# Performance work log

Hardware: AMD Instinct MI355X
Metric: run time of the kernel (lower is better)

Reference implementation:

```python
import jax, jax.numpy as jnp
import numpy as np

B, N, F_IN, F_OUT, T, E, K = 8, 1024, 32, 64, 24, 16384, 3


def setup_inputs() -> dict:
    key = jax.random.key(0)
    ks = jax.random.split(key, 9)
    return {
        "x": jax.random.normal(ks[0], (B, N, F_IN, T), jnp.float32),
        "edge_index": jax.random.randint(ks[1], (2, E), 0, N),
        "edge_weight": jax.random.uniform(ks[2], (E,), jnp.float32),
        # attention params (xavier-ish scale)
        "Ve": jax.random.normal(ks[3], (T, T), jnp.float32) * 0.2,
        "be": jax.random.normal(ks[4], (1, T, T), jnp.float32) * 0.2,
        "Vs": jax.random.normal(ks[5], (N, N), jnp.float32) * 0.03,
        "bs": jax.random.normal(ks[6], (1, N, N), jnp.float32) * 0.03,
        # ChebConv: K linear layers (no bias) + shared bias
        "cheb_W": jax.random.normal(ks[7], (K, F_IN, F_OUT), jnp.float32) * (1.0 / np.sqrt(F_IN)),
        "cheb_b": jnp.zeros((F_OUT,), jnp.float32),
        # 1x1 residual Conv2d(F_IN -> F_OUT): weight (F_OUT, F_IN), bias (F_OUT,)
        "res_W": jax.random.normal(ks[8], (F_OUT, F_IN), jnp.float32) * (1.0 / np.sqrt(F_IN)),
        "res_b": jnp.zeros((F_OUT,), jnp.float32),
    }


def _cheb_conv(x, row, col, w, Wk, b):
    """PyG-style ChebConv applied to a batch of graphs sharing edges.
    x: (BT, N, Fin). Scaled Laplacian with lambda_max=2 reduces to
    L_hat = -D^{-1/2} A D^{-1/2} with zero diagonal (self-loops removed).
    """
    n = x.shape[1]
    w = jnp.where(row == col, jnp.zeros_like(w), w)  # remove_self_loops
    deg = jnp.zeros((n,), x.dtype).at[row].add(w)
    dis = jnp.where(deg > 0, jax.lax.rsqrt(jnp.where(deg > 0, deg, 1.0)), 0.0)
    norm = -dis[row] * w * dis[col]  # (E,)

    def prop(z):  # z: (BT, N, F) -> L_hat @ z
        msg = norm[None, :, None] * z[:, row, :]  # (BT, E, F)
        return jnp.zeros_like(z).at[:, col, :].add(msg)

    Tx0 = x
    out = Tx0 @ Wk[0]
    Tx1 = prop(Tx0)
    out = out + Tx1 @ Wk[1]
    for k in range(2, Wk.shape[0]):  # small fixed K, not a data-dim loop
        Tx2 = 2.0 * prop(Tx1) - Tx0
        out = out + Tx2 @ Wk[k]
        Tx0, Tx1 = Tx1, Tx2
    return out + b


def reference(x, edge_index, edge_weight, Ve, be, Vs, bs, cheb_W, cheb_b, res_W, res_b):
    b_, n, f, t = x.shape
    row, col = edge_index[0], edge_index[1]

    # --- temporal attention: E = softmax(Ve @ sigmoid(X^T X) + be) ---
    x_flat = x.reshape(b_, n * f, t)
    score_t = jnp.einsum('bmt,bmu->btu', x_flat, x_flat)
    E_att = jax.nn.softmax(jnp.einsum('tu,buv->btv', Ve, jax.nn.sigmoid(score_t)) + be, axis=-1)
    x_TA = (x_flat @ E_att).reshape(b_, n, f, t)

    # --- spatial attention: S = softmax(Vs @ sigmoid(X X^T) + bs) ---
    xr = x_TA.reshape(b_, n, f * t)
    score_s = jnp.einsum('bnd,bmd->bnm', xr, xr)
    S_att = jax.nn.softmax(jnp.einsum('nm,bmk->bnk', Vs, jax.nn.sigmoid(score_s)) + bs, axis=-1)
    x_SA = (S_att @ xr).reshape(b_, n, f, t)

    # --- Chebyshev graph conv, batched over all B*T slices at once ---
    xg = x_SA.transpose(0, 3, 1, 2).reshape(b_ * t, n, f)  # (BT, N, Fin)
    x_gcn = _cheb_conv(xg, row, col, edge_weight, cheb_W, cheb_b)
    x_gcn = x_gcn.reshape(b_, t, n, -1).transpose(0, 2, 3, 1)  # (B, N, Fout, T)

    # --- 1x1 residual conv over channel dim ---
    x_res = jnp.einsum('gf,bnft->bngt', res_W, x) + res_b[None, None, :, None]

    return jax.nn.relu(x_gcn + x_res)
```

## Files before the change

### kernel.cpp

```cpp
#include <hip/hip_runtime.h>
#include <math.h>

#define NB 1024
#define FB 32
#define TB 24
#define GB 64
#define BB 8
#define EB 16384
#define MB 32768
#define DB 768
#define BTB 192
#define WSP 6144

typedef __attribute__((ext_vector_type(8))) short sh8;
typedef __attribute__((ext_vector_type(4))) float f32x4;

__device__ __forceinline__ float wsum(float v){
  #pragma unroll
  for (int o = 32; o; o >>= 1) v += __shfl_down(v, o);
  return v;
}
__device__ __forceinline__ float wmax(float v){
  #pragma unroll
  for (int o = 32; o; o >>= 1) v = fmaxf(v, __shfl_down(v, o));
  return v;
}
__device__ __forceinline__ float sigm(float v){ return 1.f / (1.f + expf(-v)); }
__device__ __forceinline__ float b2f(unsigned short u){ unsigned int t = ((unsigned int)u) << 16; return __uint_as_float(t); }
__device__ __forceinline__ unsigned short f2b(float f){
  unsigned int u = __float_as_uint(f);
  u += 0x7fffu + ((u >> 16) & 1u);
  return (unsigned short)(u >> 16);
}
__device__ __forceinline__ void gload16(const void* g, void* l){
  typedef const __attribute__((address_space(1))) unsigned int* gp_t;
  typedef __attribute__((address_space(3))) unsigned int* lp_t;
  __builtin_amdgcn_global_load_lds((gp_t)g, (lp_t)l, 16, 0, 0);
}

__global__ __launch_bounds__(256) void k_score(const float* __restrict__ x,
                                               float* __restrict__ score){
  const int b = blockIdx.y, ch = blockIdx.x;
  __shared__ float xs[512 * 24];
  const float* src = x + (size_t)b * (MB * TB) + (size_t)ch * 512 * 24;
  #pragma unroll
  for (int p = 0; p < 12; ++p){
    int i = p * 256 + threadIdx.x;
    ((float4*)xs)[i] = ((const float4*)src)[i];
  }
  __syncthreads();
  if (threadIdx.x < 192){
    const int t = threadIdx.x >> 3, u0 = (threadIdx.x & 7) * 3;
    float a0 = 0.f, a1 = 0.f, a2 = 0.f;
    for (int m = 0; m < 512; ++m){
      const float xt = xs[m * 24 + t];
      a0 = fmaf(xt, xs[m * 24 + u0 + 0], a0);
      a1 = fmaf(xt, xs[m * 24 + u0 + 1], a1);
      a2 = fmaf(xt, xs[m * 24 + u0 + 2], a2);
    }
    float* sb = score + (size_t)b * 576 + t * 24 + u0;
    atomicAdd(sb + 0, a0); atomicAdd(sb + 1, a1); atomicAdd(sb + 2, a2);
  }
}

__global__ __launch_bounds__(64) void k_eatt(const float* __restrict__ score,
                                             const float* __restrict__ Ve,
                                             const float* __restrict__ be,
                                             float* __restrict__ Eatt){
  const int b = blockIdx.x;
  __shared__ float sg[576], Ar[576], Vel[576], bel[576];
  for (int i = threadIdx.x; i < 576; i += 64){
    sg[i] = sigm(score[(size_t)b * 576 + i]);
    Vel[i] = Ve[i]; bel[i] = be[i];
  }
  __syncthreads();
  for (int i = threadIdx.x; i < 576; i += 64){
    int t = i / 24, v = i % 24;
    float s = 0.f;
    #pragma unroll
    for (int u = 0; u < 24; ++u) s = fmaf(Vel[t*24+u], sg[u*24+v], s);
    Ar[i] = s + bel[i];
  }
  __syncthreads();
  if (threadIdx.x < 24){
    const int t = threadIdx.x;
    float mx = -1e30f;
    #pragma unroll
    for (int v = 0; v < 24; ++v) mx = fmaxf(mx, Ar[t*24+v]);
    float e[24]; float sum = 0.f;
    #pragma unroll
    for (int v = 0; v < 24; ++v){ e[v] = expf(Ar[t*24+v] - mx); sum += e[v]; }
    const float inv = 1.f / sum;
    #pragma unroll
    for (int v = 0; v < 24; ++v) Eatt[(size_t)b * 576 + t*24 + v] = e[v] * inv;
  }
}

__global__ __launch_bounds__(256) void k_xta(const float* __restrict__ x,
                                             const float* __restrict__ Eatt,
                                             unsigned short* __restrict__ xh){
  __shared__ float E[576];
  const int b = blockIdx.x >> 7;
  for (int i = threadIdx.x; i < 576; i += 256) E[i] = Eatt[(size_t)b * 576 + i];
  __syncthreads();
  const size_t m = (size_t)blockIdx.x * 256 + threadIdx.x;
  const float* xr = x + m * TB;
  float in[TB], o[TB];
  #pragma unroll
  for (int q = 0; q < 6; ++q){
    float4 v = *(const float4*)(xr + q * 4);
    in[q*4+0] = v.x; in[q*4+1] = v.y; in[q*4+2] = v.z; in[q*4+3] = v.w;
  }
  #pragma unroll
  for (int v = 0; v < TB; ++v) o[v] = 0.f;
  #pragma unroll
  for (int u = 0; u < TB; ++u){
    const float xv = in[u];
    #pragma unroll
    for (int v = 0; v < TB; ++v) o[v] = fmaf(xv, E[u*24+v], o[v]);
  }
  unsigned int pk[12];
  #pragma unroll
  for (int q = 0; q < 12; ++q)
    pk[q] = (unsigned int)f2b(o[2*q]) | ((unsigned int)f2b(o[2*q+1]) << 16);
  uint4* op = (uint4*)(xh + m * TB);
  op[0] = make_uint4(pk[0], pk[1], pk[2], pk[3]);
  op[1] = make_uint4(pk[4], pk[5], pk[6], pk[7]);
  op[2] = make_uint4(pk[8], pk[9], pk[10], pk[11]);
}

__global__ __launch_bounds__(256) void k_tr(const unsigned short* __restrict__ in,
                                            unsigned short* __restrict__ out){
  const int dt = blockIdx.x, nt = blockIdx.y, b = blockIdx.z;
  __shared__ unsigned short ts[64 * 66];
  const unsigned short* ib = in + (size_t)b * (NB * DB) + (size_t)(nt * 64) * DB + dt * 64;
  #pragma unroll
  for (int p = 0; p < 8; ++p){
    int fl = p * 256 + threadIdx.x;
    int rr = fl >> 5, cc = (fl & 31) * 2;
    unsigned int v = *(const unsigned int*)(ib + (size_t)rr * DB + cc);
    ts[rr * 66 + cc] = (unsigned short)v;
    ts[rr * 66 + cc + 1] = (unsigned short)(v >> 16);
  }
  __syncthreads();
  unsigned short* ob = out + (size_t)b * (NB * DB) + (size_t)(dt * 64) * NB + nt * 64;
  #pragma unroll
  for (int p = 0; p < 16; ++p){
    int fl = p * 256 + threadIdx.x;
    int dd = fl >> 6, nn = fl & 63;
    ob[(size_t)dd * NB + nn] = ts[nn * 66 + dd];
  }
}

template<int EPI>
__global__ __launch_bounds__(256) void k_mgemm(const unsigned short* __restrict__ A,
                                               const unsigned short* __restrict__ B,
                                               unsigned short* __restrict__ C,
                                               int lda, int ldb, int ldc, int Kk, int nbx,
                                               long sA, long sB, long sC){
  __shared__ unsigned short As[2][8192];
  __shared__ unsigned short Bs[2][8192];
  const int d = blockIdx.x;
  const int bz = d & 7;
  const int rr = d >> 3;
  const int bx = rr % nbx, by = rr / nbx;
  A += (size_t)bz * sA; B += (size_t)bz * sB; C += (size_t)bz * sC;
  const int i0 = by * 128, j0 = bx * 128;
  const int tid = threadIdx.x, wave = tid >> 6, lane = tid & 63;
  const int fr = lane & 15, rowb = (lane >> 4) * 4;
  const int wr = (wave >> 1) * 64, wc = (wave & 1) * 64;
  const int srow = tid >> 3;
  const int sko = (((lane & 7) ^ (lane >> 3)) * 8);
  f32x4 acc[4][4];
  #pragma unroll
  for (int m = 0; m < 4; ++m)
    #pragma unroll
    for (int n = 0; n < 4; ++n) acc[m][n] = 0.f;

  auto stage = [&](int buf, int k0){
    #pragma unroll
    for (int it = 0; it < 4; ++it){
      const int r = it * 32 + srow;
      gload16(A + (size_t)(i0 + r) * lda + k0 + sko, &As[buf][(it*4 + wave) * 512]);
      gload16(B + (size_t)(j0 + r) * ldb + k0 + sko, &Bs[buf][(it*4 + wave) * 512]);
    }
  };
  auto compute = [&](int buf){
    #pragma unroll
    for (int kk = 0; kk < 2; ++kk){
      const int ch = kk * 4 + (lane >> 4);
      const int cs = (ch ^ (fr & 7)) * 8;
      sh8 af[4], bfr[4];
      #pragma unroll
      for (int m = 0; m < 4; ++m)
        af[m] = *(const sh8*)&As[buf][(wr + m*16 + fr) * 64 + cs];
      #pragma unroll
      for (int n = 0; n < 4; ++n)
        bfr[n] = *(const sh8*)&Bs[buf][(wc + n*16 + fr) * 64 + cs];
      #pragma unroll
      for (int m = 0; m < 4; ++m)
        #pragma unroll
        for (int n = 0; n < 4; ++n)
          acc[m][n] = __builtin_amdgcn_mfma_f32_16x16x32_bf16(af[m], bfr[n], acc[m][n], 0, 0, 0);
    }
  };

  stage(0, 0);
  asm volatile("s_waitcnt vmcnt(0)" ::: "memory");
  __builtin_amdgcn_s_barrier();
  int cur = 0;
  for (int k0 = 64; k0 < Kk; k0 += 64){
    stage(cur ^ 1, k0);
    compute(cur);
    asm volatile("s_waitcnt vmcnt(0)" ::: "memory");
    __builtin_amdgcn_s_barrier();
    cur ^= 1;
  }
  compute(cur);

  #pragma unroll
  for (int m = 0; m < 4; ++m){
    const int row = i0 + wr + m*16 + rowb;
    #pragma unroll
    for (int n = 0; n < 4; ++n){
      const int colg = j0 + wc + n*16 + fr;
      #pragma unroll
      for (int r = 0; r < 4; ++r){
        float v = acc[m][n][r];
        if (EPI == 1) v = sigm(v);
        C[(size_t)(row + r) * ldc + colg] = f2b(v);
      }
    }
  }
}

__global__ __launch_bounds__(256) void k_softmax_s(const unsigned short* __restrict__ C2h,
                                                   const float* __restrict__ bs,
                                                   unsigned short* __restrict__ Sh){
  const int blk = blockIdx.x;
  const int n = blk & 1023;
  const unsigned short* row = C2h + (size_t)blk * 1024;
  const float* bsr = bs + (size_t)n * 1024;
  const int tid = threadIdx.x;
  uint2 rv = ((const uint2*)row)[tid];
  float4 bb = ((const float4*)bsr)[tid];
  float v0 = b2f((unsigned short)rv.x)         + bb.x;
  float v1 = b2f((unsigned short)(rv.x >> 16)) + bb.y;
  float v2 = b2f((unsigned short)rv.y)         + bb.z;
  float v3 = b2f((unsigned short)(rv.y >> 16)) + bb.w;
  float mx = fmaxf(fmaxf(v0, v1), fmaxf(v2, v3));
  mx = wmax(mx);
  __shared__ float s4[4];
  __shared__ float s4b[4];
  if ((tid & 63) == 0) s4[tid >> 6] = mx;
  __syncthreads();
  mx = fmaxf(fmaxf(s4[0], s4[1]), fmaxf(s4[2], s4[3]));
  float e0 = expf(v0 - mx), e1 = expf(v1 - mx), e2 = expf(v2 - mx), e3 = expf(v3 - mx);
  float sum = wsum(e0 + e1 + e2 + e3);
  if ((tid & 63) == 0) s4b[tid >> 6] = sum;
  __syncthreads();
  sum = s4b[0] + s4b[1] + s4b[2] + s4b[3];
  const float inv = 1.f / sum;
  uint2 ov;
  ov.x = (unsigned int)f2b(e0 * inv) | ((unsigned int)f2b(e1 * inv) << 16);
  ov.y = (unsigned int)f2b(e2 * inv) | ((unsigned int)f2b(e3 * inv) << 16);
  ((uint2*)(Sh + (size_t)blk * 1024))[tid] = ov;
}

__global__ __launch_bounds__(256) void k_t0n(const unsigned short* __restrict__ xSAh,
                                             unsigned short* __restrict__ T0n){
  const int n0 = blockIdx.x * 8, b = blockIdx.y;
  __shared__ unsigned short s[8 * 32 * 25];
  const unsigned int* src = (const unsigned int*)(xSAh + ((size_t)b * NB + n0) * DB);
  #pragma unroll
  for (int p = 0; p < 12; ++p){
    int i = p * 256 + threadIdx.x;
    unsigned int v = src[i];
    int d0 = (i * 2) % DB, nn = (i * 2) / DB;
    int f0 = d0 / 24, t0 = d0 % 24;
    int d1 = d0 + 1, f1 = d1 / 24, t1 = d1 % 24;
    s[(nn * 32 + f0) * 25 + t0] = (unsigned short)v;
    s[(nn * 32 + f1) * 25 + t1] = (unsigned short)(v >> 16);
  }
  __syncthreads();
  #pragma unroll
  for (int nn = 0; nn < 8; ++nn){
    unsigned short* dst = T0n + ((size_t)(n0 + nn) * BTB + b * TB) * FB;
    #pragma unroll
    for (int p = 0; p < 3; ++p){
      int i2 = p * 256 + threadIdx.x;
      int t = i2 >> 5, f = i2 & 31;
      dst[t * FB + f] = s[(nn * 32 + f) * 25 + t];
    }
  }
}

__global__ __launch_bounds__(256) void k_xtn(const float* __restrict__ x,
                                             unsigned short* __restrict__ xTn){
  const int n0 = blockIdx.x * 8, b = blockIdx.y;
  __shared__ float xl[8 * 32 * 25];
  const float* src = x + ((size_t)b * NB + n0) * DB;
  #pragma unroll
  for (int p = 0; p < 24; ++p){
    int i = p * 256 + threadIdx.x;
    int n = i / 768, rem = i % 768, f = rem / 24, t = rem % 24;
    xl[(n * 32 + f) * 25 + t] = src[i];
  }
  __syncthreads();
  #pragma unroll
  for (int nn = 0; nn < 8; ++nn){
    unsigned short* dst = xTn + ((size_t)(n0 + nn) * BTB + b * TB) * FB;
    #pragma unroll
    for (int p = 0; p < 3; ++p){
      int i2 = p * 256 + threadIdx.x;
      int t = i2 >> 5, f = i2 & 31;
      dst[t * FB + f] = f2b(xl[(nn * 32 + f) * 25 + t]);
    }
  }
}

__global__ __launch_bounds__(256) void k_edge_deg(const int* __restrict__ ei,
                                                  const float* __restrict__ ew,
                                                  float* __restrict__ deg,
                                                  int* __restrict__ cnt){
  int e = blockIdx.x * 256 + threadIdx.x;
  if (e >= EB) return;
  int r = ei[e], c = ei[EB + e];
  float w = (r == c) ? 0.f : ew[e];
  atomicAdd(&deg[r], w);
  atomicAdd(&cnt[c], 1);
}

__global__ __launch_bounds__(1024) void k_scan(const int* __restrict__ cnt,
                                               int* __restrict__ ptr,
                                               int* __restrict__ fill){
  __shared__ int sd[1024];
  const int i = threadIdx.x;
  int c = cnt[i];
  sd[i] = c;
  __syncthreads();
  int v = c;
  for (int s = 1; s < 1024; s <<= 1){
    int t = (i >= s) ? sd[i - s] : 0;
    __syncthreads();
    v += t; sd[i] = v;
    __syncthreads();
  }
  ptr[i + 1] = v;
  fill[i] = v - c;
  if (i == 0) ptr[0] = 0;
}

__global__ __launch_bounds__(256) void k_edge_fill(const int* __restrict__ ei,
                                                   const float* __restrict__ ew,
                                                   const float* __restrict__ deg,
                                                   int* __restrict__ fill,
                                                   int* __restrict__ cidx,
                                                   float* __restrict__ normv){
  int e = blockIdx.x * 256 + threadIdx.x;
  if (e >= EB) return;
  int r = ei[e], c = ei[EB + e];
  float w = (r == c) ? 0.f : ew[e];
  float dr = deg[r], dc = deg[c];
  float ir = dr > 0.f ? rsqrtf(dr) : 0.f;
  float ic = dc > 0.f ? rsqrtf(dc) : 0.f;
  normv[e] = -ir * w * ic;
  int pos = atomicAdd(&fill[c], 1);
  cidx[pos] = e;
}

#define ACC8(vv) { \
  acc[0] = fmaf(w, b2f((unsigned short)(vv).x), acc[0]); \
  acc[1] = fmaf(w, b2f((unsigned short)((vv).x >> 16)), acc[1]); \
  acc[2] = fmaf(w, b2f((unsigned short)(vv).y), acc[2]); \
  acc[3] = fmaf(w, b2f((unsigned short)((vv).y >> 16)), acc[3]); \
  acc[4] = fmaf(w, b2f((unsigned short)(vv).z), acc[4]); \
  acc[5] = fmaf(w, b2f((unsigned short)((vv).z >> 16)), acc[5]); \
  acc[6] = fmaf(w, b2f((unsigned short)(vv).w), acc[6]); \
  acc[7] = fmaf(w, b2f((unsigned short)((vv).w >> 16)), acc[7]); }

__global__ __launch_bounds__(256) void k_spmm(const unsigned short* __restrict__ z,
                                              const float* __restrict__ normv,
                                              const int* __restrict__ cidx,
                                              const int* __restrict__ ei,
                                              const int* __restrict__ ptr,
                                              const unsigned short* __restrict__ sub,
                                              float scale,
                                              unsigned short* __restrict__ outz){
  const int c = blockIdx.x & 1023;
  const int off = (blockIdx.x >> 10) * 2048 + threadIdx.x * 8;
  const int j0 = ptr[c], j1 = ptr[c + 1];
  __shared__ int rs[128];
  __shared__ float ws[128];
  float acc[8];
  #pragma unroll
  for (int q = 0; q < 8; ++q) acc[q] = 0.f;
  for (int jb = j0; jb < j1; jb += 128){
    const int cnt = min(128, j1 - jb);
    __syncthreads();
    for (int j = threadIdx.x; j < cnt; j += 256){
      int e = cidx[jb + j];
      rs[j] = ei[e];
      ws[j] = normv[e];
    }
    __syncthreads();
    for (int j = 0; j < cnt; ++j){
      const uint4 v = *(const uint4*)(z + (size_t)rs[j] * WSP + off);
      const float w = ws[j];
      ACC8(v)
    }
  }
  float sv[8];
  if (sub){
    const uint4 s0 = *(const uint4*)(sub + (size_t)c * WSP + off);
    sv[0]=b2f((unsigned short)s0.x); sv[1]=b2f((unsigned short)(s0.x>>16));
    sv[2]=b2f((unsigned short)s0.y); sv[3]=b2f((unsigned short)(s0.y>>16));
    sv[4]=b2f((unsigned short)s0.z); sv[5]=b2f((unsigned short)(s0.z>>16));
    sv[6]=b2f((unsigned short)s0.w); sv[7]=b2f((unsigned short)(s0.w>>16));
  } else {
    #pragma unroll
    for (int q = 0; q < 8; ++q) sv[q] = 0.f;
  }
  unsigned int pk[4];
  #pragma unroll
  for (int q = 0; q < 4; ++q){
    float a = scale * acc[2*q]     - sv[2*q];
    float b = scale * acc[2*q + 1] - sv[2*q + 1];
    pk[q] = (unsigned int)f2b(a) | ((unsigned int)f2b(b) << 16);
  }
  *(uint4*)(outz + (size_t)c * WSP + off) = make_uint4(pk[0], pk[1], pk[2], pk[3]);
}

__global__ __launch_bounds__(256) void k_fgemm(const unsigned short* __restrict__ T0n,
                                               const unsigned short* __restrict__ T1n,
                                               const unsigned short* __restrict__ T2n,
                                               const unsigned short* __restrict__ xTn,
                                               const unsigned short* __restrict__ Wh,
                                               const float* __restrict__ bsum,
                                               float* __restrict__ out){
  __shared__ unsigned short As[16384];
  __shared__ unsigned short Ws[8192];
  const int m0 = blockIdx.x * 128;
  const int tid = threadIdx.x, wave = tid >> 6, lane = tid & 63;
  const int fr = lane & 15, rowb = (lane >> 4) * 4;
  const int wr = (wave >> 1) * 64, wc = (wave & 1) * 32;
  #pragma unroll
  for (int it = 0; it < 8; ++it){
    const int row = it * 16 + wave * 4 + (lane >> 4);
    const int g = (lane & 15) ^ (row & 7);
    const int ss = g >> 2, off = (g & 3) * 8;
    const unsigned short* bp = (ss == 0) ? T0n : (ss == 1) ? T1n : (ss == 2) ? T2n : xTn;
    gload16(bp + (size_t)(m0 + row) * FB + off, &As[(it*4 + wave) * 512]);
  }
  #pragma unroll
  for (int it = 0; it < 4; ++it){
    const int row = it * 16 + wave * 4 + (lane >> 4);
    const int g = (lane & 15) ^ (row & 7);
    gload16(Wh + (size_t)row * 128 + g * 8, &Ws[(it*4 + wave) * 512]);
  }
  __syncthreads();
  f32x4 acc[4][2];
  #pragma unroll
  for (int m = 0; m < 4; ++m){ acc[m][0] = 0.f; acc[m][1] = 0.f; }
  #pragma unroll
  for (int kk = 0; kk < 4; ++kk){
    const int ch = kk * 4 + (lane >> 4);
    const int cs = (ch ^ (fr & 7)) * 8;
    sh8 af[4], bf2[2];
    #pragma unroll
    for (int m = 0; m < 4; ++m)
      af[m] = *(const sh8*)&As[(wr + m*16 + fr) * 128 + cs];
    #pragma unroll
    for (int n = 0; n < 2; ++n)
      bf2[n] = *(const sh8*)&Ws[(wc + n*16 + fr) * 128 + cs];
    #pragma unroll
    for (int m = 0; m < 4; ++m)
      #pragma unroll
      for (int n = 0; n < 2; ++n)
        acc[m][n] = __builtin_amdgcn_mfma_f32_16x16x32_bf16(af[m], bf2[n], acc[m][n], 0, 0, 0);
  }
  #pragma unroll
  for (int m = 0; m < 4; ++m){
    const int row4 = m0 + wr + m*16 + rowb;
    const int nn = row4 / 192;
    const int rem = row4 - nn * 192;
    const int b = rem / 24;
    const int t0 = rem - b * 24;
    #pragma unroll
    for (int n = 0; n < 2; ++n){
      const int g = wc + n*16 + fr;
      const float bv = bsum[g];
      float4 v;
      v.x = fmaxf(acc[m][n][0] + bv, 0.f);
      v.y = fmaxf(acc[m][n][1] + bv, 0.f);
      v.z = fmaxf(acc[m][n][2] + bv, 0.f);
      v.w = fmaxf(acc[m][n][3] + bv, 0.f);
      *(float4*)(out + (((size_t)b * NB + nn) * GB + g) * TB + t0) = v;
    }
  }
}

__global__ __launch_bounds__(256) void k_vsh(const float* __restrict__ Vs,
                                             unsigned short* __restrict__ Vsh){
  int i = (blockIdx.x * 256 + threadIdx.x) * 4;
  float4 v = *(const float4*)(Vs + i);
  unsigned short* o = Vsh + i;
  o[0] = f2b(v.x); o[1] = f2b(v.y); o[2] = f2b(v.z); o[3] = f2b(v.w);
}

__global__ __launch_bounds__(256) void k_wcat(const float* __restrict__ cW,
                                              const float* __restrict__ cB,
                                              const float* __restrict__ rW,
                                              const float* __restrict__ rB,
                                              unsigned short* __restrict__ Wh,
                                              float* __restrict__ bsum){
  for (int i = threadIdx.x; i < 8192; i += 256){
    int g = i >> 7, k = i & 127;
    int s = k >> 5, f = k & 31;
    float v = (s < 3) ? cW[(s * 32 + f) * 64 + g] : rW[g * 32 + f];
    Wh[i] = f2b(v);
  }
  if (threadIdx.x < 64) bsum[threadIdx.x] = cB[threadIdx.x] + rB[threadIdx.x];
}

extern "C" void kernel_launch(void* const* d_in, const int* in_sizes, int n_in,
                              void* d_out, int out_size, void* d_ws, size_t ws_size,
                              hipStream_t stream){
  const float* x  = (const float*)d_in[0];
  const int*   ei = (const int*)d_in[1];
  const float* ew = (const float*)d_in[2];
  const float* Ve = (const float*)d_in[3];
  const float* be = (const float*)d_in[4];
  const float* Vs = (const float*)d_in[5];
  const float* bs = (const float*)d_in[6];
  const float* cW = (const float*)d_in[7];
  const float* cB = (const float*)d_in[8];
  const float* rW = (const float*)d_in[9];
  const float* rB = (const float*)d_in[10];
  float* out = (float*)d_out;

  char* W = (char*)d_ws;
  unsigned short* sigh  = (unsigned short*)(W + 0);
  unsigned short* Sh    = sigh;
  unsigned short* xTAh  = (unsigned short*)(W + 16777216);
  unsigned short* T0n   = xTAh;
  unsigned short* xTAhT = (unsigned short*)(W + 29360128);
  unsigned short* T1n   = xTAhT;
  unsigned short* xTn   = (unsigned short*)(W + 41943040);
  unsigned short* xSAh  = (unsigned short*)(W + 54525952);
  unsigned short* T2n   = xSAh;
  unsigned short* C2h   = (unsigned short*)(W + 67108864);
  unsigned short* Vsh   = (unsigned short*)(W + 83886080);
  unsigned short* Wh    = (unsigned short*)(W + 92274688);
  float* bsum  = (float*)(W + 92291072);
  float* score = (float*)(W + 92291328);
  float* Eatt  = (float*)(W + 92309760);
  float* normv = (float*)(W + 92328192);
  float* deg   = (float*)(W + 92393728);
  int*   cnt   = (int*)(W + 92397824);
  int*   ptr   = (int*)(W + 92401920);
  int*   fill  = (int*)(W + 92406272);
  int*   cidx  = (int*)(W + 92410368);

  hipMemsetAsync(score, 0, 18432, stream);
  hipMemsetAsync(deg, 0, 8192, stream);

  k_wcat<<<1, 256, 0, stream>>>(cW, cB, rW, rB, Wh, bsum);
  k_vsh<<<1024, 256, 0, stream>>>(Vs, Vsh);
  k_xtn<<<dim3(128, 8), 256, 0, stream>>>(x, xTn);

  k_score<<<dim3(64, 8), 256, 0, stream>>>(x, score);
  k_eatt<<<8, 64, 0, stream>>>(score, Ve, be, Eatt);
  k_xta<<<1024, 256, 0, stream>>>(x, Eatt, xTAh);
  k_tr<<<dim3(12, 16, 8), 256, 0, stream>>>(xTAh, xTAhT);

  k_mgemm<1><<<512, 256, 0, stream>>>(xTAh, xTAh, sigh, DB, DB, NB, DB, 8,
                                      (long)NB*DB, (long)NB*DB, (long)NB*NB);
  k_mgemm<2><<<512, 256, 0, stream>>>(Vsh, sigh, C2h, NB, NB, NB, NB, 8,
                                      0L, (long)NB*NB, (long)NB*NB);
  k_softmax_s<<<8192, 256, 0, stream>>>(C2h, bs, Sh);
  k_mgemm<2><<<384, 256, 0, stream>>>(Sh, xTAhT, xSAh, NB, NB, DB, NB, 6,
                                      (long)NB*NB, (long)NB*DB, (long)NB*DB);

  k_t0n<<<dim3(128, 8), 256, 0, stream>>>(xSAh, T0n);
  k_edge_deg<<<64, 256, 0, stream>>>(ei, ew, deg, cnt);
  k_scan<<<1, 1024, 0, stream>>>(cnt, ptr, fill);
  k_edge_fill<<<64, 256, 0, stream>>>(ei, ew, deg, fill, cidx, normv);
  k_spmm<<<3072, 256, 0, stream>>>(T0n, normv, cidx, ei, ptr, nullptr, 1.f, T1n);
  k_spmm<<<3072, 256, 0, stream>>>(T1n, normv, cidx, ei, ptr, T0n, 2.f, T2n);

  k_fgemm<<<1536, 256, 0, stream>>>(T0n, T1n, T2n, xTn, Wh, bsum, out);
}
```

Measured before the change: 235.2 us.

## Fuse temporal score with x transpose pass and read bf16 xTn for x_TA

Merges the kernel that builds the bf16 transposed copy of x with the temporal score kernel, so x is read from global memory once for both outputs. The x_TA kernel now reads the half-size bf16 xTn buffer instead of fp32 x, which cuts input traffic. In exchange, x_TA is computed from bf16-rounded inputs rather than fp32, a small precision loss. The score kernel also grows from 64 to 128 blocks per batch, each covering 256 rows, which doubles the number of score atomics.

After: 237.1 us. No clear change (+0.8%).

```diff
diff --git a/kernel.cpp b/kernel.cpp
--- a/kernel.cpp
+++ b/kernel.cpp
@@ -38,25 +38,37 @@
   __builtin_amdgcn_global_load_lds((gp_t)g, (lp_t)l, 16, 0, 0);
 }
 
-__global__ __launch_bounds__(256) void k_score(const float* __restrict__ x,
+__global__ __launch_bounds__(256) void k_pass1(const float* __restrict__ x,
+                                               unsigned short* __restrict__ xTn,
                                                float* __restrict__ score){
-  const int b = blockIdx.y, ch = blockIdx.x;
-  __shared__ float xs[512 * 24];
-  const float* src = x + (size_t)b * (MB * TB) + (size_t)ch * 512 * 24;
-  #pragma unroll
-  for (int p = 0; p < 12; ++p){
+  const int n0 = blockIdx.x * 8, b = blockIdx.y;
+  __shared__ float xl[8 * 32 * 25];
+  const float* src = x + ((size_t)b * NB + n0) * DB;
+  #pragma unroll
+  for (int p = 0; p < 24; ++p){
     int i = p * 256 + threadIdx.x;
-    ((float4*)xs)[i] = ((const float4*)src)[i];
-  }
-  __syncthreads();
+    int n = i / 768, rem = i % 768, f = rem / 24, t = rem % 24;
+    xl[(n * 32 + f) * 25 + t] = src[i];
+  }
+  __syncthreads();
+  #pragma unroll
+  for (int nn = 0; nn < 8; ++nn){
+    unsigned short* dst = xTn + ((size_t)(n0 + nn) * BTB + b * TB) * FB;
+    #pragma unroll
+    for (int p = 0; p < 3; ++p){
+      int i2 = p * 256 + threadIdx.x;
+      int t = i2 >> 5, f = i2 & 31;
+      dst[t * FB + f] = f2b(xl[(nn * 32 + f) * 25 + t]);
+    }
+  }
   if (threadIdx.x < 192){
     const int t = threadIdx.x >> 3, u0 = (threadIdx.x & 7) * 3;
     float a0 = 0.f, a1 = 0.f, a2 = 0.f;
-    for (int m = 0; m < 512; ++m){
-      const float xt = xs[m * 24 + t];
-      a0 = fmaf(xt, xs[m * 24 + u0 + 0], a0);
-      a1 = fmaf(xt, xs[m * 24 + u0 + 1], a1);
-      a2 = fmaf(xt, xs[m * 24 + u0 + 2], a2);
+    for (int m = 0; m < 256; ++m){
+      const float xt = xl[m * 25 + t];
+      a0 = fmaf(xt, xl[m * 25 + u0 + 0], a0);
+      a1 = fmaf(xt, xl[m * 25 + u0 + 1], a1);
+      a2 = fmaf(xt, xl[m * 25 + u0 + 2], a2);
     }
     float* sb = score + (size_t)b * 576 + t * 24 + u0;
     atomicAdd(sb + 0, a0); atomicAdd(sb + 1, a1); atomicAdd(sb + 2, a2);
@@ -96,21 +108,28 @@
   }
 }
 
-__global__ __launch_bounds__(256) void k_xta(const float* __restrict__ x,
-                                             const float* __restrict__ Eatt,
-                                             unsigned short* __restrict__ xh){
+__global__ __launch_bounds__(256) void k_xta2(const unsigned short* __restrict__ xTn,
+                                              const float* __restrict__ Eatt,
+                                              unsigned short* __restrict__ xTAh){
+  const int n0 = blockIdx.x * 8, b = blockIdx.y;
   __shared__ float E[576];
-  const int b = blockIdx.x >> 7;
+  __shared__ unsigned short xl[8 * 32 * 25];
   for (int i = threadIdx.x; i < 576; i += 256) E[i] = Eatt[(size_t)b * 576 + i];
-  __syncthreads();
-  const size_t m = (size_t)blockIdx.x * 256 + threadIdx.x;
-  const float* xr = x + m * TB;
+  #pragma unroll
+  for (int p = 0; p < 12; ++p){
+    int i = p * 256 + threadIdx.x;
+    int nn = i / 384, within = i % 384;
+    unsigned int v = *(const unsigned int*)(xTn + ((size_t)(n0 + nn) * BTB + b * TB) * FB + within * 2);
+    int e0 = within * 2, t0 = e0 >> 5, f0 = e0 & 31;
+    int e1 = e0 + 1,     t1 = e1 >> 5, f1 = e1 & 31;
+    xl[(nn * 32 + f0) * 25 + t0] = (unsigned short)v;
+    xl[(nn * 32 + f1) * 25 + t1] = (unsigned short)(v >> 16);
+  }
+  __syncthreads();
+  const int r = threadIdx.x;
   float in[TB], o[TB];
   #pragma unroll
-  for (int q = 0; q < 6; ++q){
-    float4 v = *(const float4*)(xr + q * 4);
-    in[q*4+0] = v.x; in[q*4+1] = v.y; in[q*4+2] = v.z; in[q*4+3] = v.w;
-  }
+  for (int u = 0; u < TB; ++u) in[u] = b2f(xl[r * 25 + u]);
   #pragma unroll
   for (int v = 0; v < TB; ++v) o[v] = 0.f;
   #pragma unroll
@@ -123,7 +142,7 @@
   #pragma unroll
   for (int q = 0; q < 12; ++q)
     pk[q] = (unsigned int)f2b(o[2*q]) | ((unsigned int)f2b(o[2*q+1]) << 16);
-  uint4* op = (uint4*)(xh + m * TB);
+  uint4* op = (uint4*)(xTAh + ((size_t)b * MB + n0 * 32 + r) * TB);
   op[0] = make_uint4(pk[0], pk[1], pk[2], pk[3]);
   op[1] = make_uint4(pk[4], pk[5], pk[6], pk[7]);
   op[2] = make_uint4(pk[8], pk[9], pk[10], pk[11]);
@@ -291,30 +310,6 @@
       int i2 = p * 256 + threadIdx.x;
       int t = i2 >> 5, f = i2 & 31;
       dst[t * FB + f] = s[(nn * 32 + f) * 25 + t];
-    }
-  }
-}
-
-__global__ __launch_bounds__(256) void k_xtn(const float* __restrict__ x,
-                                             unsigned short* __restrict__ xTn){
-  const int n0 = blockIdx.x * 8, b = blockIdx.y;
-  __shared__ float xl[8 * 32 * 25];
-  const float* src = x + ((size_t)b * NB + n0) * DB;
-  #pragma unroll
-  for (int p = 0; p < 24; ++p){
-    int i = p * 256 + threadIdx.x;
-    int n = i / 768, rem = i % 768, f = rem / 24, t = rem % 24;
-    xl[(n * 32 + f) * 25 + t] = src[i];
-  }
-  __syncthreads();
-  #pragma unroll
-  for (int nn = 0; nn < 8; ++nn){
-    unsigned short* dst = xTn + ((size_t)(n0 + nn) * BTB + b * TB) * FB;
-    #pragma unroll
-    for (int p = 0; p < 3; ++p){
-      int i2 = p * 256 + threadIdx.x;
-      int t = i2 >> 5, f = i2 & 31;
-      dst[t * FB + f] = f2b(xl[(nn * 32 + f) * 25 + t]);
     }
   }
 }
@@ -567,11 +562,10 @@
 
   k_wcat<<<1, 256, 0, stream>>>(cW, cB, rW, rB, Wh, bsum);
   k_vsh<<<1024, 256, 0, stream>>>(Vs, Vsh);
-  k_xtn<<<dim3(128, 8), 256, 0, stream>>>(x, xTn);
-
-  k_score<<<dim3(64, 8), 256, 0, stream>>>(x, score);
+
+  k_pass1<<<dim3(128, 8), 256, 0, stream>>>(x, xTn, score);
   k_eatt<<<8, 64, 0, stream>>>(score, Ve, be, Eatt);
-  k_xta<<<1024, 256, 0, stream>>>(x, Eatt, xTAh);
+  k_xta2<<<dim3(128, 8), 256, 0, stream>>>(xTn, Eatt, xTAh);
   k_tr<<<dim3(12, 16, 8), 256, 0, stream>>>(xTAh, xTAhT);
 
   k_mgemm<1><<<512, 256, 0, stream>>>(xTAh, xTAh, sigh, DB, DB, NB, DB, 8,
```
